# Kernel tuning notes

Measured on AMD Instinct MI355X. Metric: run time of the kernel, lower is better.

The kernel has to match this reference:

```python
import jax, jax.numpy as jnp
import numpy as np

B, T, D, U = 128, 256, 256, 1024


def setup_inputs() -> dict:
    key = jax.random.key(0)
    ks = jax.random.split(key, 5)
    features = jax.random.normal(ks[0], (B, T, D), dtype=jnp.float32)
    # irregular positive time deltas in (0, 1)
    time_steps = jax.random.uniform(ks[1], (B, T), dtype=jnp.float32)
    scale_x = 1.0 / np.sqrt(D)
    scale_h = 1.0 / np.sqrt(U)
    Wx = jax.random.normal(ks[2], (D, 2 * U), dtype=jnp.float32) * scale_x
    Wh = jax.random.normal(ks[3], (U, 2 * U), dtype=jnp.float32) * scale_h
    b = jnp.zeros((2 * U,), dtype=jnp.float32)
    w_tau = jax.random.uniform(ks[4], (U,), dtype=jnp.float32)
    h0 = jnp.zeros((B, U), dtype=jnp.float32)
    return {"features": features, "time_steps": time_steps, "Wx": Wx,
            "Wh": Wh, "b": b, "w_tau": w_tau, "h0": h0}


def reference(features, time_steps, Wx, Wh, b, w_tau, h0):
    """IrregularRNN with exact closed-form LTC cell, return_sequences=True.

    Per step: f = sigmoid(pre_f), A = tanh(pre_a),
              h' = (h - A) * exp(-dt * (softplus(w_tau) + f)) + A
    """
    tau = jax.nn.softplus(w_tau)  # [U]

    def step(h, xt):
        x_t, dt_t = xt                      # [B,D], [B]
        pre = x_t @ Wx + h @ Wh + b         # [B,2U]
        f = jax.nn.sigmoid(pre[:, :U])
        a = jnp.tanh(pre[:, U:])
        decay = jnp.exp(-dt_t[:, None] * (tau + f))
        h_new = (h - a) * decay + a
        return h_new, h_new

    xs = (jnp.swapaxes(features, 0, 1), jnp.swapaxes(time_steps, 0, 1))
    _, ys = jax.lax.scan(step, h0, xs)      # ys: [T,B,U]
    return jnp.swapaxes(ys, 0, 1)           # [B,T,U]
```

## Files before the change

### kernel.cpp

```cpp
#include <hip/hip_runtime.h>

typedef _Float16 v8h  __attribute__((ext_vector_type(8)));
typedef _Float16 v4h  __attribute__((ext_vector_type(4)));
typedef float    v4f  __attribute__((ext_vector_type(4)));
typedef unsigned int u32x4 __attribute__((ext_vector_type(4)));

#define BATCH   128
#define TSTEPS  256
#define DFEAT   256
#define UDIM    1024
#define KTOT    1280
#define NCOL    2048
#define ASTRIDE 1288


__global__ __launch_bounds__(1024)
void ltc_rnn_kernel(const float* __restrict__ features,
                    const float* __restrict__ tsteps,
                    const float* __restrict__ Wx,
                    const float* __restrict__ Wh,
                    const float* __restrict__ bias,
                    const float* __restrict__ wtau,
                    const float* __restrict__ h0,
                    float* __restrict__ out,
                    unsigned* __restrict__ counters,
                    _Float16* __restrict__ hbufs)
{
  __shared__ _Float16 Alds[16 * ASTRIDE];
  __shared__ float    Plds[16 * 64 * 4];
  __shared__ _Float16 Hout[16][32];
  __shared__ float    OutT[16][32];
  __shared__ float    dtlds[2][16];

  const int tid  = threadIdx.x;
  const int w    = tid >> 6;
  const int lane = tid & 63;
  const int n    = lane & 15;
  const int q    = lane >> 4;
  const int cg   = w & 3;
  const int ks   = w >> 2;
  const int g    = blockIdx.x & 7;
  const int cb   = blockIdx.x >> 3;
  const int u0   = cb * 32;

  const int gcol = (n < 8) ? (u0 + cg * 8 + n) : (UDIM + u0 + cg * 8 + (n - 8));
  v8h bfr[10];
  #pragma unroll
  for (int c = 0; c < 10; ++c) {
    #pragma unroll
    for (int j = 0; j < 8; ++j) {
      const int k = ks * 320 + c * 32 + q * 8 + j;
      const float wv = (k < DFEAT) ? Wx[(size_t)k * NCOL + gcol]
                                   : Wh[(size_t)(k - DFEAT) * NCOL + gcol];
      bfr[c][j] = (_Float16)wv;
    }
  }

  const float bias_own = bias[gcol];
  const int   u_lane   = u0 + cg * 8 + (n & 7);
  const float tau      = logf(1.0f + __expf(wtau[u_lane]));

  float h_reg[4];
  #pragma unroll
  for (int i = 0; i < 4; ++i)
    h_reg[i] = h0[(size_t)(g * 16 + q * 4 + i) * UDIM + u_lane];

  if (tid < 16) dtlds[0][tid] = tsteps[(size_t)(g * 16 + tid) * TSTEPS + 0];
  {
    const int r = tid >> 6, k4 = tid & 63;
    v4f x4 = *(const v4f*)(features + (size_t)(g * 16 + r) * (TSTEPS * DFEAT) + k4 * 4);
    v4h xh = {(_Float16)x4.x, (_Float16)x4.y, (_Float16)x4.z, (_Float16)x4.w};
    *(v4h*)&Alds[r * ASTRIDE + k4 * 4] = xh;
    #pragma unroll
    for (int jj = 0; jj < 4; ++jj) {
      const int c = tid + jj * 1024, hr = c >> 8, hk4 = c & 255;
      v4f h4 = *(const v4f*)(h0 + (size_t)(g * 16 + hr) * UDIM + hk4 * 4);
      v4h hh = {(_Float16)h4.x, (_Float16)h4.y, (_Float16)h4.z, (_Float16)h4.w};
      *(v4h*)&Alds[hr * ASTRIDE + DFEAT + hk4 * 4] = hh;
    }
  }
  __syncthreads();

  for (int t = 0; t < TSTEPS; ++t) {
    _Float16* hdst = hbufs + ((t + 1) & 1) * (BATCH * UDIM);

    {
      v4f acc = {0.f, 0.f, 0.f, 0.f};
      const _Float16* abase = &Alds[n * ASTRIDE + ks * 320 + q * 8];
      #pragma unroll
      for (int c = 0; c < 10; ++c) {
        v8h a = *(const v8h*)(abase + c * 32);
        acc = __builtin_amdgcn_mfma_f32_16x16x32_f16(a, bfr[c], acc, 0, 0, 0);
      }
      *(v4f*)&Plds[(w * 64 + lane) * 4] = acc;
    }
    __syncthreads();

    if (w < 4) {
      v4f p = *(v4f*)&Plds[((0 * 4 + w) * 64 + lane) * 4];
      #pragma unroll
      for (int s = 1; s < 4; ++s) {
        v4f ps = *(v4f*)&Plds[((s * 4 + w) * 64 + lane) * 4];
        p.x += ps.x; p.y += ps.y; p.z += ps.z; p.w += ps.w;
      }
      float pf[4], pa[4];
      #pragma unroll
      for (int i = 0; i < 4; ++i) {
        const float v = p[i] + bias_own;
        const float o = __shfl_xor(v, 8);
        pf[i] = v; pa[i] = o;
      }
      if (n < 8) {
        #pragma unroll
        for (int i = 0; i < 4; ++i) {
          const int   row_l = q * 4 + i;
          const float dt    = dtlds[t & 1][row_l];
          const float f     = 1.0f / (1.0f + __expf(-pf[i]));
          const float av    = 2.0f / (1.0f + __expf(-2.0f * pa[i])) - 1.0f;
          const float decay = __expf(-dt * (tau + f));
          const float hn    = (h_reg[i] - av) * decay + av;
          h_reg[i] = hn;
          Hout[row_l][cg * 8 + n] = (_Float16)hn;
          OutT[row_l][cg * 8 + n] = hn;
        }
      }
    }
    __syncthreads();

    if (t + 1 < TSTEPS) {
      if (tid < 16) dtlds[(t + 1) & 1][tid] = tsteps[(size_t)(g * 16 + tid) * TSTEPS + t + 1];
      const int r = tid >> 6, k4 = tid & 63;
      v4f x4 = *(const v4f*)(features + (size_t)(g * 16 + r) * (TSTEPS * DFEAT)
                             + (size_t)(t + 1) * DFEAT + k4 * 4);
      v4h xh = {(_Float16)x4.x, (_Float16)x4.y, (_Float16)x4.z, (_Float16)x4.w};
      *(v4h*)&Alds[r * ASTRIDE + k4 * 4] = xh;
    }

    if (tid < 64) {
      const int row = tid >> 2, c8 = tid & 3;
      v8h hv = *(v8h*)&Hout[row][c8 * 8];
      _Float16* dp = hdst + (size_t)(g * 16 + row) * UDIM + u0 + c8 * 8;
      asm volatile("global_store_dwordx4 %0, %1, off sc0 sc1\n\t"
                   "s_waitcnt vmcnt(0)"
                   :: "v"(dp), "v"(__builtin_bit_cast(u32x4, hv)) : "memory");
    } else if (tid < 192) {
      const int row = (tid - 64) >> 3, c4 = (tid - 64) & 7;
      v4f ov = *(v4f*)&OutT[row][c4 * 4];
      *(v4f*)(out + (size_t)(g * 16 + row) * (TSTEPS * UDIM)
              + (size_t)t * UDIM + u0 + c4 * 4) = ov;
    }
    __syncthreads();

    if (t + 1 < TSTEPS) {
      if (tid == 0) {
        __hip_atomic_fetch_add(&counters[g * 64], 1u, __ATOMIC_RELAXED,
                               __HIP_MEMORY_SCOPE_AGENT);
        const unsigned tgt = 32u * (unsigned)(t + 1);
        while (__hip_atomic_load(&counters[g * 64], __ATOMIC_RELAXED,
                                 __HIP_MEMORY_SCOPE_AGENT) < tgt)
          __builtin_amdgcn_s_sleep(1);
      }
      __syncthreads();

      const _Float16* hsrc = hbufs + ((t + 1) & 1) * (BATCH * UDIM);
      const int c0 = tid, c1 = tid + 1024;
      const _Float16* p0 = hsrc + (size_t)(g * 16 + (c0 >> 7)) * UDIM + (c0 & 127) * 8;
      const _Float16* p1 = hsrc + (size_t)(g * 16 + (c1 >> 7)) * UDIM + (c1 & 127) * 8;
      u32x4 r0, r1;
      asm volatile("global_load_dwordx4 %0, %2, off sc0 sc1\n\t"
                   "global_load_dwordx4 %1, %3, off sc0 sc1\n\t"
                   "s_waitcnt vmcnt(0)"
                   : "=v"(r0), "=v"(r1) : "v"(p0), "v"(p1) : "memory");
      *(v8h*)&Alds[(c0 >> 7) * ASTRIDE + DFEAT + (c0 & 127) * 8] = __builtin_bit_cast(v8h, r0);
      *(v8h*)&Alds[(c1 >> 7) * ASTRIDE + DFEAT + (c1 & 127) * 8] = __builtin_bit_cast(v8h, r1);
      __syncthreads();
    }
  }
}

extern "C" void kernel_launch(void* const* d_in, const int* in_sizes, int n_in,
                              void* d_out, int out_size, void* d_ws, size_t ws_size,
                              hipStream_t stream) {
  const float* features = (const float*)d_in[0];
  const float* tsamp    = (const float*)d_in[1];
  const float* Wx       = (const float*)d_in[2];
  const float* Wh       = (const float*)d_in[3];
  const float* bias     = (const float*)d_in[4];
  const float* wtau     = (const float*)d_in[5];
  const float* h0       = (const float*)d_in[6];
  float*     out      = (float*)d_out;
  unsigned*  counters = (unsigned*)d_ws;
  _Float16*  hbufs    = (_Float16*)((char*)d_ws + 4096);

  hipMemsetAsync(d_ws, 0, 4096, stream);
  hipLaunchKernelGGL(ltc_rnn_kernel, dim3(256), dim3(1024), 0, stream,
                     features, tsamp, Wx, Wh, bias, wtau, h0, out, counters, hbufs);
}
```

Measured before the change: 1.122 ms.

## Replace atomic counter barrier with per-block flags and wave-parallel polling

Replaces the per-group atomic counter grid barrier with per-block step flags. Wave 0 publishes its hidden slice and then sets its flag, while all 64 lanes poll the 32 peer flags in parallel using a ballot. The barrier is merged into a single __syncthreads per step, and the fp32 output is written straight from registers, so the OutT staging buffer goes away. The goal is lower cross-block synchronization latency per timestep. The trade-off is memory ordering: the flag store issues after a waited data store, with no explicit release fence.

```diff
diff --git a/kernel.cpp b/kernel.cpp
--- a/kernel.cpp
+++ b/kernel.cpp
@@ -9,7 +9,6 @@
 #define TSTEPS  256
 #define DFEAT   256
 #define UDIM    1024
-#define KTOT    1280
 #define NCOL    2048
 #define ASTRIDE 1288
 
@@ -23,13 +22,12 @@
                     const float* __restrict__ wtau,
                     const float* __restrict__ h0,
                     float* __restrict__ out,
-                    unsigned* __restrict__ counters,
+                    unsigned* __restrict__ flags,
                     _Float16* __restrict__ hbufs)
 {
   __shared__ _Float16 Alds[16 * ASTRIDE];
   __shared__ float    Plds[16 * 64 * 4];
   __shared__ _Float16 Hout[16][32];
-  __shared__ float    OutT[16][32];
   __shared__ float    dtlds[2][16];
 
   const int tid  = threadIdx.x;
@@ -82,6 +80,7 @@
   __syncthreads();
 
   for (int t = 0; t < TSTEPS; ++t) {
+    const bool more = (t + 1 < TSTEPS);
     _Float16* hdst = hbufs + ((t + 1) & 1) * (BATCH * UDIM);
 
     {
@@ -96,6 +95,7 @@
     }
     __syncthreads();
 
+    float outv[4];
     if (w < 4) {
       v4f p = *(v4f*)&Plds[((0 * 4 + w) * 64 + lane) * 4];
       #pragma unroll
@@ -120,14 +120,35 @@
           const float decay = __expf(-dt * (tau + f));
           const float hn    = (h_reg[i] - av) * decay + av;
           h_reg[i] = hn;
-          Hout[row_l][cg * 8 + n] = (_Float16)hn;
-          OutT[row_l][cg * 8 + n] = hn;
+          outv[i]  = hn;
+          Hout[row_l][w * 8 + n] = (_Float16)hn;
         }
       }
     }
     __syncthreads();
 
-    if (t + 1 < TSTEPS) {
+    if (w == 0 && more) {
+      const int row = lane >> 2, c8 = lane & 3;
+      v8h hv = *(v8h*)&Hout[row][c8 * 8];
+      _Float16* dp = hdst + (size_t)(g * 16 + row) * UDIM + u0 + c8 * 8;
+      asm volatile("global_store_dwordx4 %0, %1, off sc0 sc1\n\t"
+                   "s_waitcnt vmcnt(0)"
+                   :: "v"(dp), "v"(__builtin_bit_cast(u32x4, hv)) : "memory");
+      if (lane == 0) {
+        unsigned tg = (unsigned)(t + 1);
+        asm volatile("global_store_dword %0, %1, off sc0 sc1"
+                     :: "v"(&flags[g * 64 + cb]), "v"(tg) : "memory");
+      }
+    }
+
+    if (w < 4 && n < 8) {
+      #pragma unroll
+      for (int i = 0; i < 4; ++i) {
+        const int row = g * 16 + q * 4 + i;
+        out[(size_t)row * (TSTEPS * UDIM) + (size_t)t * UDIM + u_lane] = outv[i];
+      }
+    }
+    if (more) {
       if (tid < 16) dtlds[(t + 1) & 1][tid] = tsteps[(size_t)(g * 16 + tid) * TSTEPS + t + 1];
       const int r = tid >> 6, k4 = tid & 63;
       v4f x4 = *(const v4f*)(features + (size_t)(g * 16 + r) * (TSTEPS * DFEAT)
@@ -136,32 +157,20 @@
       *(v4h*)&Alds[r * ASTRIDE + k4 * 4] = xh;
     }
 
-    if (tid < 64) {
-      const int row = tid >> 2, c8 = tid & 3;
-      v8h hv = *(v8h*)&Hout[row][c8 * 8];
-      _Float16* dp = hdst + (size_t)(g * 16 + row) * UDIM + u0 + c8 * 8;
-      asm volatile("global_store_dwordx4 %0, %1, off sc0 sc1\n\t"
-                   "s_waitcnt vmcnt(0)"
-                   :: "v"(dp), "v"(__builtin_bit_cast(u32x4, hv)) : "memory");
-    } else if (tid < 192) {
-      const int row = (tid - 64) >> 3, c4 = (tid - 64) & 7;
-      v4f ov = *(v4f*)&OutT[row][c4 * 4];
-      *(v4f*)(out + (size_t)(g * 16 + row) * (TSTEPS * UDIM)
-              + (size_t)t * UDIM + u0 + c4 * 4) = ov;
+    if (w == 0 && more) {
+      const unsigned* fp = &flags[g * 64 + (lane & 31)];
+      const unsigned  tg = (unsigned)t;
+      for (;;) {
+        unsigned v;
+        asm volatile("global_load_dword %0, %1, off sc0 sc1\n\t"
+                     "s_waitcnt vmcnt(0)"
+                     : "=v"(v) : "v"(fp) : "memory");
+        if (__ballot(v <= tg) == 0ull) break;
+      }
     }
     __syncthreads();
 
-    if (t + 1 < TSTEPS) {
-      if (tid == 0) {
-        __hip_atomic_fetch_add(&counters[g * 64], 1u, __ATOMIC_RELAXED,
-                               __HIP_MEMORY_SCOPE_AGENT);
-        const unsigned tgt = 32u * (unsigned)(t + 1);
-        while (__hip_atomic_load(&counters[g * 64], __ATOMIC_RELAXED,
-                                 __HIP_MEMORY_SCOPE_AGENT) < tgt)
-          __builtin_amdgcn_s_sleep(1);
-      }
-      __syncthreads();
-
+    if (more) {
       const _Float16* hsrc = hbufs + ((t + 1) & 1) * (BATCH * UDIM);
       const int c0 = tid, c1 = tid + 1024;
       const _Float16* p0 = hsrc + (size_t)(g * 16 + (c0 >> 7)) * UDIM + (c0 & 127) * 8;
@@ -188,11 +197,11 @@
   const float* bias     = (const float*)d_in[4];
   const float* wtau     = (const float*)d_in[5];
   const float* h0       = (const float*)d_in[6];
-  float*     out      = (float*)d_out;
-  unsigned*  counters = (unsigned*)d_ws;
-  _Float16*  hbufs    = (_Float16*)((char*)d_ws + 4096);
+  float*     out    = (float*)d_out;
+  unsigned*  flags  = (unsigned*)d_ws;
+  _Float16*  hbufs  = (_Float16*)((char*)d_ws + 4096);
 
   hipMemsetAsync(d_ws, 0, 4096, stream);
   hipLaunchKernelGGL(ltc_rnn_kernel, dim3(256), dim3(1024), 0, stream,
-                     features, tsamp, Wx, Wh, bias, wtau, h0, out, counters, hbufs);
+                     features, tsamp, Wx, Wh, bias, wtau, h0, out, flags, hbufs);
 }
```

After: 1.028 ms. 1.09x faster.
